# Optimization experiments

Measured on AMD Instinct MI355X. Metric: run time of the kernel, lower is better.

## Reference

```python
import jax, jax.numpy as jnp
import numpy as np

S, B, C = 1024, 2, 20
COORD, NOOBJ, NPRED = 5.0, 0.5, 5


def setup_inputs() -> dict:
    key = jax.random.key(0)
    k1, k2, k3 = jax.random.split(key, 3)
    pred = jax.random.normal(k1, (S, S, B * NPRED + C), dtype=jnp.float32)
    # target: box part uniform in [0,1) (w,h must be >=0 for sqrt), classes one-hot
    box_t = jax.random.uniform(k2, (S, S, B * NPRED), dtype=jnp.float32)
    cls_idx = jax.random.randint(k3, (S, S), 0, C)
    cls_t = jax.nn.one_hot(cls_idx, C, dtype=jnp.float32)
    target = jnp.concatenate([box_t, cls_t], axis=-1)
    return {"pred": pred, "target": target}


def reference(pred, target):
    # boxes: [S, S, B, 5] with (conf, x, y, w, h)
    boxes_p = pred[..., : B * NPRED].reshape(S, S, B, NPRED)
    boxes_t = target[..., : B * NPRED].reshape(S, S, B, NPRED)

    conf_p, x_p, y_p = boxes_p[..., 0], boxes_p[..., 1], boxes_p[..., 2]
    w_p = jnp.sqrt(jnp.abs(boxes_p[..., 3]))
    h_p = jnp.sqrt(jnp.abs(boxes_p[..., 4]))

    conf_t, x_t, y_t = boxes_t[..., 0], boxes_t[..., 1], boxes_t[..., 2]
    w_t = jnp.sqrt(boxes_t[..., 3])
    h_t = jnp.sqrt(boxes_t[..., 4])

    xy_loss = jnp.sum((jnp.square(x_t - x_p) + jnp.square(y_t - y_p)) * conf_t)
    box_loss = jnp.sum((jnp.square(w_t - w_p) + jnp.square(h_t - h_p)) * conf_t)
    conf_sq = jnp.square(conf_t - conf_p)
    confidence_loss = jnp.sum(conf_sq * conf_t)
    noobj_confidence_loss = jnp.sum(conf_sq * (1.0 - conf_t))

    # class loss: only cells whose target class vector sums to exactly 1.0
    pred_cls = pred[..., B * NPRED :].reshape(S * S, C)
    tgt_cls = target[..., B * NPRED :].reshape(S * S, C)
    cell_mask = (jnp.sum(tgt_cls, axis=-1) == 1.0).astype(pred.dtype)  # [S*S]
    per_cell = jnp.sum(jnp.square(tgt_cls) - jnp.square(pred_cls), axis=-1)
    cls_loss = jnp.sum(per_cell * cell_mask)

    return COORD * xy_loss + COORD * box_loss + confidence_loss + noobj_confidence_loss + cls_loss
```

## Files before the change

kernel.cpp:

```cpp
#include <hip/hip_runtime.h>


constexpr int S_DIM       = 1024;
constexpr int NCELL       = S_DIM * S_DIM;
constexpr int CH          = 30;
constexpr int BLOCK       = 256;
constexpr int TILE_CELLS  = 128;
constexpr int TILE_FLOATS = TILE_CELLS * CH;
constexpr int TILE_F4     = TILE_FLOATS / 4;
constexpr int NTILES      = NCELL / TILE_CELLS;
constexpr int GRID        = 2048;

__device__ __forceinline__ float wave_reduce_sum(float v) {
#pragma unroll
    for (int off = 32; off > 0; off >>= 1)
        v += __shfl_down(v, off, 64);
    return v;
}

__global__ __launch_bounds__(BLOCK, 5) void yolo_partial_kernel(
        const float* __restrict__ pred,
        const float* __restrict__ tgt,
        float* __restrict__ partial) {
    __shared__ float sp[TILE_FLOATS];
    __shared__ float st[TILE_FLOATS];

    const int tid  = threadIdx.x;
    const int cell = tid >> 1;
    const int half = tid & 1;
    float acc = 0.0f;

    for (int tile = blockIdx.x; tile < NTILES; tile += GRID) {
        const float4* gp = reinterpret_cast<const float4*>(pred) + (size_t)tile * TILE_F4;
        const float4* gt = reinterpret_cast<const float4*>(tgt)  + (size_t)tile * TILE_F4;
        float4* s4p = reinterpret_cast<float4*>(sp);
        float4* s4t = reinterpret_cast<float4*>(st);

        __syncthreads();
#pragma unroll
        for (int j = 0; j < 3; ++j) {
            const int idx = j * BLOCK + tid;
            s4p[idx] = gp[idx];
            s4t[idx] = gt[idx];
        }
        {
            const int idx = 3 * BLOCK + tid;
            if (idx < TILE_F4) { s4p[idx] = gp[idx]; s4t[idx] = gt[idx]; }
        }
        __syncthreads();

        const float* pp = sp + cell * CH;
        const float* tt = st + cell * CH;

        {
            const int o = 5 * half;
            const float conf_p = pp[o + 0];
            const float x_p    = pp[o + 1];
            const float y_p    = pp[o + 2];
            const float w_p    = sqrtf(fabsf(pp[o + 3]));
            const float h_p    = sqrtf(fabsf(pp[o + 4]));
            const float conf_t = tt[o + 0];
            const float x_t    = tt[o + 1];
            const float y_t    = tt[o + 2];
            const float w_t    = sqrtf(tt[o + 3]);
            const float h_t    = sqrtf(tt[o + 4]);

            const float dx = x_t - x_p, dy = y_t - y_p;
            const float dw = w_t - w_p, dh = h_t - h_p;
            const float dc = conf_t - conf_p;

            acc += 5.0f * ((dx * dx + dy * dy) * conf_t)
                 + 5.0f * ((dw * dw + dh * dh) * conf_t)
                 + dc * dc;
        }

        float ssum = 0.0f, per_cell = 0.0f;
        const int co = 10 + 10 * half;
#pragma unroll
        for (int k = 0; k < 10; ++k) {
            const float tc = tt[co + k];
            const float pc = pp[co + k];
            ssum     += tc;
            per_cell += tc * tc - pc * pc;
        }
        const float tot = ssum + __shfl_xor(ssum, 1, 64);
        acc += (tot == 1.0f) ? per_cell : 0.0f;
    }

    __shared__ float red[BLOCK / 64];
    const int lane = tid & 63;
    const int wid  = tid >> 6;

    float v = wave_reduce_sum(acc);
    if (lane == 0) red[wid] = v;
    __syncthreads();
    if (wid == 0) {
        v = (lane < (BLOCK / 64)) ? red[lane] : 0.0f;
        v = wave_reduce_sum(v);
        if (lane == 0) partial[blockIdx.x] = v;
    }
}

__global__ __launch_bounds__(256) void yolo_final_kernel(
        const float* __restrict__ partial,
        float* __restrict__ out,
        int n) {
    float acc = 0.0f;
    for (int i = threadIdx.x; i < n; i += 256)
        acc += partial[i];

    __shared__ float red[4];
    const int lane = threadIdx.x & 63;
    const int wid  = threadIdx.x >> 6;
    float v = wave_reduce_sum(acc);
    if (lane == 0) red[wid] = v;
    __syncthreads();
    if (wid == 0) {
        v = (lane < 4) ? red[lane] : 0.0f;
        v = wave_reduce_sum(v);
        if (lane == 0) out[0] = v;
    }
}

extern "C" void kernel_launch(void* const* d_in, const int* in_sizes, int n_in,
                              void* d_out, int out_size, void* d_ws, size_t ws_size,
                              hipStream_t stream) {
    const float* pred = (const float*)d_in[0];
    const float* tgt  = (const float*)d_in[1];
    float* out        = (float*)d_out;
    float* partial    = (float*)d_ws;

    yolo_partial_kernel<<<GRID, BLOCK, 0, stream>>>(pred, tgt, partial);
    yolo_final_kernel<<<1, 256, 0, stream>>>(partial, out, GRID);
}
```

Measured before the change: 45.21 us.

## Register-prefetch next tile and make each wave own its LDS slice without block barriers

Each wave now loads and stages its own 32-cell slice of the tile in LDS, so the block-wide __syncthreads around staging is dropped in favour of wave-local lgkmcnt waits. The global loads for the next tile are issued into registers before computing the current one, overlapping memory latency with compute. The final block reduction is replaced by per-wave partials, and the final kernel now sums four times as many values. Register-held prefetch buffers raise register pressure, and the occupancy hint is lowered from 5 to 4.

```diff
diff --git a/kernel.cpp b/kernel.cpp
--- a/kernel.cpp
+++ b/kernel.cpp
@@ -1,15 +1,15 @@
 #include <hip/hip_runtime.h>
 
 
-constexpr int S_DIM       = 1024;
-constexpr int NCELL       = S_DIM * S_DIM;
-constexpr int CH          = 30;
-constexpr int BLOCK       = 256;
-constexpr int TILE_CELLS  = 128;
-constexpr int TILE_FLOATS = TILE_CELLS * CH;
-constexpr int TILE_F4     = TILE_FLOATS / 4;
-constexpr int NTILES      = NCELL / TILE_CELLS;
-constexpr int GRID        = 2048;
+constexpr int S_DIM      = 1024;
+constexpr int NCELL      = S_DIM * S_DIM;
+constexpr int CH         = 30;
+constexpr int BLOCK      = 256;
+constexpr int TILE_CELLS = 128;
+constexpr int TILE_F4    = TILE_CELLS * CH / 4;
+constexpr int WAVE_F4    = TILE_F4 / 4;
+constexpr int NTILES     = NCELL / TILE_CELLS;
+constexpr int GRID       = 2048;
 
 __device__ __forceinline__ float wave_reduce_sum(float v) {
 #pragma unroll
@@ -18,39 +18,59 @@
     return v;
 }
 
-__global__ __launch_bounds__(BLOCK, 5) void yolo_partial_kernel(
+__global__ __launch_bounds__(BLOCK, 4) void yolo_partial_kernel(
         const float* __restrict__ pred,
         const float* __restrict__ tgt,
         float* __restrict__ partial) {
-    __shared__ float sp[TILE_FLOATS];
-    __shared__ float st[TILE_FLOATS];
+    __shared__ float4 smem4[2 * TILE_F4];
+    float* s = reinterpret_cast<float*>(smem4);
 
     const int tid  = threadIdx.x;
-    const int cell = tid >> 1;
-    const int half = tid & 1;
+    const int wv   = tid >> 6;
+    const int ln   = tid & 63;
+    const int half = ln & 1;
+    const int cl   = ln >> 1;
+
+    const float4* gp4 = reinterpret_cast<const float4*>(pred);
+    const float4* gt4 = reinterpret_cast<const float4*>(tgt);
+
+    const int pbase = wv * (WAVE_F4 * 4) + cl * CH;
+    const int tbase = TILE_F4 * 4 + wv * (WAVE_F4 * 4) + cl * CH;
+    const int lbase = wv * WAVE_F4 + ln;
+
+    float4 rp[4], rt[4];
+
+    int tile = blockIdx.x;
+    {
+        const size_t g = (size_t)tile * TILE_F4 + wv * WAVE_F4 + ln;
+#pragma unroll
+        for (int j = 0; j < 4; ++j)
+            if (j * 64 + ln < WAVE_F4) { rp[j] = gp4[g + j * 64]; rt[j] = gt4[g + j * 64]; }
+    }
+
     float acc = 0.0f;
+    for (; tile < NTILES; tile += GRID) {
+        asm volatile("s_waitcnt lgkmcnt(0)" ::: "memory");
 
-    for (int tile = blockIdx.x; tile < NTILES; tile += GRID) {
-        const float4* gp = reinterpret_cast<const float4*>(pred) + (size_t)tile * TILE_F4;
-        const float4* gt = reinterpret_cast<const float4*>(tgt)  + (size_t)tile * TILE_F4;
-        float4* s4p = reinterpret_cast<float4*>(sp);
-        float4* s4t = reinterpret_cast<float4*>(st);
+#pragma unroll
+        for (int j = 0; j < 4; ++j)
+            if (j * 64 + ln < WAVE_F4) {
+                smem4[lbase + j * 64]           = rp[j];
+                smem4[TILE_F4 + lbase + j * 64] = rt[j];
+            }
 
-        __syncthreads();
+        const int ntile = tile + GRID;
+        if (ntile < NTILES) {
+            const size_t g = (size_t)ntile * TILE_F4 + wv * WAVE_F4 + ln;
 #pragma unroll
-        for (int j = 0; j < 3; ++j) {
-            const int idx = j * BLOCK + tid;
-            s4p[idx] = gp[idx];
-            s4t[idx] = gt[idx];
+            for (int j = 0; j < 4; ++j)
+                if (j * 64 + ln < WAVE_F4) { rp[j] = gp4[g + j * 64]; rt[j] = gt4[g + j * 64]; }
         }
-        {
-            const int idx = 3 * BLOCK + tid;
-            if (idx < TILE_F4) { s4p[idx] = gp[idx]; s4t[idx] = gt[idx]; }
-        }
-        __syncthreads();
 
-        const float* pp = sp + cell * CH;
-        const float* tt = st + cell * CH;
+        asm volatile("s_waitcnt lgkmcnt(0)" ::: "memory");
+
+        const float* pp = s + pbase;
+        const float* tt = s + tbase;
 
         {
             const int o = 5 * half;
@@ -74,31 +94,23 @@
                  + dc * dc;
         }
 
-        float ssum = 0.0f, per_cell = 0.0f;
-        const int co = 10 + 10 * half;
+        {
+            float ssum = 0.0f, per_cell = 0.0f;
+            const int co = 10 + 10 * half;
 #pragma unroll
-        for (int k = 0; k < 10; ++k) {
-            const float tc = tt[co + k];
-            const float pc = pp[co + k];
-            ssum     += tc;
-            per_cell += tc * tc - pc * pc;
+            for (int k = 0; k < 10; ++k) {
+                const float tc = tt[co + k];
+                const float pc = pp[co + k];
+                ssum     += tc;
+                per_cell += tc * tc - pc * pc;
+            }
+            const float tot = ssum + __shfl_xor(ssum, 1, 64);
+            acc += (tot == 1.0f) ? per_cell : 0.0f;
         }
-        const float tot = ssum + __shfl_xor(ssum, 1, 64);
-        acc += (tot == 1.0f) ? per_cell : 0.0f;
     }
 
-    __shared__ float red[BLOCK / 64];
-    const int lane = tid & 63;
-    const int wid  = tid >> 6;
-
     float v = wave_reduce_sum(acc);
-    if (lane == 0) red[wid] = v;
-    __syncthreads();
-    if (wid == 0) {
-        v = (lane < (BLOCK / 64)) ? red[lane] : 0.0f;
-        v = wave_reduce_sum(v);
-        if (lane == 0) partial[blockIdx.x] = v;
-    }
+    if (ln == 0) partial[wv * GRID + blockIdx.x] = v;
 }
 
 __global__ __launch_bounds__(256) void yolo_final_kernel(
@@ -131,5 +143,5 @@
     float* partial    = (float*)d_ws;
 
     yolo_partial_kernel<<<GRID, BLOCK, 0, stream>>>(pred, tgt, partial);
-    yolo_final_kernel<<<1, 256, 0, stream>>>(partial, out, GRID);
+    yolo_final_kernel<<<1, 256, 0, stream>>>(partial, out, 4 * GRID);
 }
```

Result: slower. 129.0 us (+185.3%).

## Double-buffer tile loads through registers and shrink grid to 512 blocks

Applied to the files above, without the earlier changes.

Adds a software pipeline: each wave prefetches the next tile's pred/target float4 chunks into registers before computing on the current LDS buffer, then stores them into the alternate LDS buffer. Work is split unevenly across waves (8/8/7/7 chunks of 64 float4). This is meant to hide global load latency behind compute and cut one barrier per tile. The grid drops to 512 blocks with a fixed iteration count, and the occupancy hint is removed. In exchange, register pressure and LDS use double, which may lower occupancy.

```diff
diff --git a/kernel.cpp b/kernel.cpp
--- a/kernel.cpp
+++ b/kernel.cpp
@@ -1,15 +1,14 @@
 #include <hip/hip_runtime.h>
 
 
-constexpr int S_DIM       = 1024;
-constexpr int NCELL       = S_DIM * S_DIM;
-constexpr int CH          = 30;
-constexpr int BLOCK       = 256;
-constexpr int TILE_CELLS  = 128;
-constexpr int TILE_FLOATS = TILE_CELLS * CH;
-constexpr int TILE_F4     = TILE_FLOATS / 4;
-constexpr int NTILES      = NCELL / TILE_CELLS;
-constexpr int GRID        = 2048;
+constexpr int CH         = 30;
+constexpr int NCELL      = 1024 * 1024;
+constexpr int BLOCK      = 256;
+constexpr int TILE_CELLS = 128;
+constexpr int TILE_F4    = TILE_CELLS * CH / 4;
+constexpr int GRID       = 512;
+constexpr int NTILES     = NCELL / TILE_CELLS;
+constexpr int NIT        = NTILES / GRID;
 
 __device__ __forceinline__ float wave_reduce_sum(float v) {
 #pragma unroll
@@ -18,39 +17,68 @@
     return v;
 }
 
-__global__ __launch_bounds__(BLOCK, 5) void yolo_partial_kernel(
+__global__ __launch_bounds__(BLOCK) void yolo_partial_kernel(
         const float* __restrict__ pred,
         const float* __restrict__ tgt,
         float* __restrict__ partial) {
-    __shared__ float sp[TILE_FLOATS];
-    __shared__ float st[TILE_FLOATS];
+    __shared__ float4 sbuf[2][2 * TILE_F4];
 
     const int tid  = threadIdx.x;
+    const int wv   = tid >> 6;
+    const int ln   = tid & 63;
     const int cell = tid >> 1;
     const int half = tid & 1;
+
+    const float4* pf4 = reinterpret_cast<const float4*>(pred);
+    const float4* tf4 = reinterpret_cast<const float4*>(tgt);
+
+    const int c0 = (wv < 2) ? wv * 8 : 16 + (wv - 2) * 7;
+
+    float4 r[8];
+
+    auto load_tile = [&](int tile) {
+        const size_t tb = (size_t)tile * TILE_F4;
+        if (wv < 2) {
+#pragma unroll
+            for (int k = 0; k < 8; ++k) {
+                const int ci = (c0 + k) * 64;
+                r[k] = (ci < TILE_F4) ? pf4[tb + ci + ln]
+                                      : tf4[tb + (ci - TILE_F4) + ln];
+            }
+        } else {
+#pragma unroll
+            for (int k = 0; k < 7; ++k) {
+                const int ci = (c0 + k) * 64;
+                r[k] = tf4[tb + (ci - TILE_F4) + ln];
+            }
+        }
+    };
+    auto store_tile = [&](int b) {
+        if (wv < 2) {
+#pragma unroll
+            for (int k = 0; k < 8; ++k) sbuf[b][(c0 + k) * 64 + ln] = r[k];
+        } else {
+#pragma unroll
+            for (int k = 0; k < 7; ++k) sbuf[b][(c0 + k) * 64 + ln] = r[k];
+        }
+    };
+
+    int t = blockIdx.x;
+    load_tile(t);
+    store_tile(0);
+    __syncthreads();
+
     float acc = 0.0f;
+    for (int it = 0; it < NIT; ++it) {
+        const int cur = it & 1;
+        const bool havenext = (it + 1 < NIT);
 
-    for (int tile = blockIdx.x; tile < NTILES; tile += GRID) {
-        const float4* gp = reinterpret_cast<const float4*>(pred) + (size_t)tile * TILE_F4;
-        const float4* gt = reinterpret_cast<const float4*>(tgt)  + (size_t)tile * TILE_F4;
-        float4* s4p = reinterpret_cast<float4*>(sp);
-        float4* s4t = reinterpret_cast<float4*>(st);
+        if (havenext) load_tile(t + GRID);
+        __builtin_amdgcn_sched_barrier(0);
 
-        __syncthreads();
-#pragma unroll
-        for (int j = 0; j < 3; ++j) {
-            const int idx = j * BLOCK + tid;
-            s4p[idx] = gp[idx];
-            s4t[idx] = gt[idx];
-        }
-        {
-            const int idx = 3 * BLOCK + tid;
-            if (idx < TILE_F4) { s4p[idx] = gp[idx]; s4t[idx] = gt[idx]; }
-        }
-        __syncthreads();
-
-        const float* pp = sp + cell * CH;
-        const float* tt = st + cell * CH;
+        const float* bf = reinterpret_cast<const float*>(&sbuf[cur][0]);
+        const float* pp = bf + cell * CH;
+        const float* tt = bf + TILE_F4 * 4 + cell * CH;
 
         {
             const int o = 5 * half;
@@ -74,30 +102,33 @@
                  + dc * dc;
         }
 
-        float ssum = 0.0f, per_cell = 0.0f;
-        const int co = 10 + 10 * half;
+        {
+            float ssum = 0.0f, per_cell = 0.0f;
+            const int co = 10 + 10 * half;
 #pragma unroll
-        for (int k = 0; k < 10; ++k) {
-            const float tc = tt[co + k];
-            const float pc = pp[co + k];
-            ssum     += tc;
-            per_cell += tc * tc - pc * pc;
+            for (int k = 0; k < 10; ++k) {
+                const float tc = tt[co + k];
+                const float pc = pp[co + k];
+                ssum     += tc;
+                per_cell += tc * tc - pc * pc;
+            }
+            const float tot = ssum + __shfl_xor(ssum, 1, 64);
+            acc += (tot == 1.0f) ? per_cell : 0.0f;
         }
-        const float tot = ssum + __shfl_xor(ssum, 1, 64);
-        acc += (tot == 1.0f) ? per_cell : 0.0f;
+
+        if (havenext) store_tile(cur ^ 1);
+        __syncthreads();
+        t += GRID;
     }
 
     __shared__ float red[BLOCK / 64];
-    const int lane = tid & 63;
-    const int wid  = tid >> 6;
-
     float v = wave_reduce_sum(acc);
-    if (lane == 0) red[wid] = v;
+    if (ln == 0) red[wv] = v;
     __syncthreads();
-    if (wid == 0) {
-        v = (lane < (BLOCK / 64)) ? red[lane] : 0.0f;
+    if (wv == 0) {
+        v = (ln < (BLOCK / 64)) ? red[ln] : 0.0f;
         v = wave_reduce_sum(v);
-        if (lane == 0) partial[blockIdx.x] = v;
+        if (ln == 0) partial[blockIdx.x] = v;
     }
 }
 
```

New measurement: 101.0 us. 2.23x slower.
